# Kernel tuning notes

Measured on AMD Instinct MI355X. Metric: run time of the kernel, lower is better.

## Reference

```python
import jax, jax.numpy as jnp
import numpy as np
from jax import lax

B, NPB = 4, 100000
N = B * NPB
C_BEV, C = 256, 64
H = W = 180
S = 10          # NUM_SWEEPS
MAXI = 64       # gt_boxes.shape[1] (max instances per sample)
NUMLOC = B * MAXI * S
NUMINST = B * MAXI
PC_MIN = -54.0
CELL = 0.075 * 8  # voxel * bev_image_stride


def setup_inputs() -> dict:
    key = jax.random.key(0)
    ks = jax.random.split(key, 20)
    pb = jnp.repeat(jnp.arange(B), NPB).astype(jnp.float32)
    xy = jax.random.uniform(ks[0], (N, 2), minval=-54.0, maxval=53.9)
    z = jax.random.uniform(ks[1], (N, 1), minval=-5.0, maxval=2.9)
    extra = jax.random.uniform(ks[2], (N, 2))
    sweep = jax.random.randint(ks[3], (N, 1), 0, S).astype(jnp.float32)
    inst = jax.random.randint(ks[4], (N, 1), 0, MAXI).astype(jnp.float32)
    points = jnp.concatenate([pb[:, None], xy, z, extra, sweep, inst, inst], axis=1)
    sc = 0.05
    return {
        'points': points,
        'spatial_features_2d': jax.random.normal(ks[5], (B, C_BEV, H, W)),
        'conv_w': jax.random.normal(ks[6], (C, C_BEV, 3, 3)) * sc,
        'bn_gamma': jnp.ones((C,)), 'bn_beta': jnp.zeros((C,)),
        'w_seg': jax.random.normal(ks[7], (C, 3)) * sc, 'b_seg': jnp.zeros((3,)),
        'w_reg': jax.random.normal(ks[8], (C, 3)) * sc, 'b_reg': jnp.zeros((3,)),
        'w_emb': jax.random.normal(ks[9], (C, 2)) * sc, 'b_emb': jnp.zeros((2,)),
        'w_shape': jax.random.normal(ks[10], (3, C)) * sc, 'b_shape': jnp.zeros((C,)),
        'w_tf': jax.random.normal(ks[11], (2 * C + 6, 7)) * sc, 'b_tf': jnp.zeros((7,)),
        'w_mos': jax.random.normal(ks[12], (C + 6, 1)) * sc, 'b_mos': jnp.zeros((1,)),
    }


def _forward(points, spatial_features_2d, conv_w, bn_gamma, bn_beta,
             w_seg, b_seg, w_reg, b_reg, w_emb, b_emb,
             w_shape, b_shape, w_tf, b_tf, w_mos, b_mos):
    # ---- shared_conv: Conv3x3 (no bias) + BatchNorm2d (training stats) + ReLU
    y = lax.conv_general_dilated(spatial_features_2d, conv_w, (1, 1), 'SAME',
                                 dimension_numbers=('NCHW', 'OIHW', 'NCHW'))
    mu = y.mean(axis=(0, 2, 3), keepdims=True)
    var = y.var(axis=(0, 2, 3), keepdims=True)
    y = (y - mu) * lax.rsqrt(var + 1e-5)
    bev = jax.nn.relu(y * bn_gamma[None, :, None, None] + bn_beta[None, :, None, None])
    bev_hwc = jnp.transpose(bev, (0, 2, 3, 1))  # [B,H,W,C]

    # ---- bilinear gather of BEV features at point locations (vectorized over batch)
    pb = points[:, 0].astype(jnp.int32)
    px = (points[:, 1] - PC_MIN) / CELL
    py = (points[:, 2] - PC_MIN) / CELL
    x0 = jnp.clip(jnp.floor(px).astype(jnp.int32), 0, W - 1)
    x1 = jnp.clip(x0 + 1, 0, W - 1)
    y0 = jnp.clip(jnp.floor(py).astype(jnp.int32), 0, H - 1)
    y1 = jnp.clip(y0 + 1, 0, H - 1)
    x0f, x1f = x0.astype(px.dtype), x1.astype(px.dtype)
    y0f, y1f = y0.astype(py.dtype), y1.astype(py.dtype)
    Ia = bev_hwc[pb, y0, x0]
    Ib = bev_hwc[pb, y1, x0]
    Ic = bev_hwc[pb, y0, x1]
    Id = bev_hwc[pb, y1, x1]
    wa = ((x1f - px) * (y1f - py))[:, None]
    wb = ((x1f - px) * (py - y0f))[:, None]
    wc = ((px - x0f) * (y1f - py))[:, None]
    wd = ((px - x0f) * (py - y0f))[:, None]
    points_feat = Ia * wa + Ib * wb + Ic * wc + Id * wd  # [N, C]

    # ---- point heads (single Linear each, mid_c=None)
    points_cls_logit = points_feat @ w_seg + b_seg
    points_offset = points_feat @ w_reg + b_reg
    points_embedding = points_feat @ w_emb + b_emb

    # ---- instance / local aggregation (training branch; all points foreground)
    sweep = points[:, 6].astype(jnp.int32)
    inst = points[:, 7].astype(jnp.int32)
    seg = (pb * MAXI + inst) * S + sweep  # dense local id in [0, NUMLOC)
    cnt = jax.ops.segment_sum(jnp.ones((N,), points.dtype), seg, NUMLOC)
    nonempty = cnt > 0
    xyz = points[:, 1:4]
    centroid = jax.ops.segment_sum(xyz, seg, NUMLOC) / jnp.clip(cnt, 1.0)[:, None]
    centered = xyz - centroid[seg]

    shape_enc = jax.ops.segment_max(centered @ w_shape + b_shape, seg, NUMLOC)
    shape_enc = jnp.where(nonempty[:, None], shape_enc, 0.0)
    locals_feat = jax.ops.segment_max(points_feat, seg, NUMLOC)
    locals_feat = jnp.where(nonempty[:, None], locals_feat, 0.0)
    locals_feat = locals_feat + shape_enc  # [NUMLOC, C]

    inst_of_local = jnp.arange(NUMLOC, dtype=jnp.int32) // S
    sweep_of_local = jnp.arange(NUMLOC, dtype=jnp.int32) % S
    neg_inf = jnp.array(-jnp.inf, locals_feat.dtype)
    globals_feat = jax.ops.segment_max(
        jnp.where(nonempty[:, None], locals_feat, neg_inf), inst_of_local, NUMINST)
    inst_nonempty = jax.ops.segment_max(nonempty, inst_of_local, NUMINST)
    globals_feat = jnp.where(inst_nonempty[:, None], globals_feat, 0.0)

    max_sweep = jax.ops.segment_max(jnp.where(nonempty, sweep_of_local, -1), inst_of_local, NUMINST)
    min_sweep = jax.ops.segment_min(jnp.where(nonempty, sweep_of_local, S), inst_of_local, NUMINST)
    inst_ids = jnp.arange(NUMINST, dtype=jnp.int32)
    idx_max = jnp.clip(inst_ids * S + max_sweep, 0, NUMLOC - 1)
    idx_min = jnp.clip(inst_ids * S + min_sweep, 0, NUMLOC - 1)
    init_center = centroid[idx_min]    # [NUMINST, 3]
    target_center = centroid[idx_max]  # [NUMINST, 3]

    locals_cat = jnp.concatenate(
        [locals_feat, globals_feat[inst_of_local], centroid, target_center[inst_of_local]], axis=1)
    locals_tf = locals_cat @ w_tf + b_tf  # [NUMLOC, 7]
    inst_feat = jnp.concatenate([globals_feat, init_center, target_center], axis=1)
    inst_mos = inst_feat @ w_mos + b_mos  # [NUMINST, 1]

    return points_cls_logit, points_offset, points_embedding, locals_tf, inst_mos


def reference(points, spatial_features_2d, conv_w, bn_gamma, bn_beta,
              w_seg, b_seg, w_reg, b_reg, w_emb, b_emb,
              w_shape, b_shape, w_tf, b_tf, w_mos, b_mos):
    return _forward(points, spatial_features_2d, conv_w, bn_gamma, bn_beta,
                    w_seg, b_seg, w_reg, b_reg, w_emb, b_emb,
                    w_shape, b_shape, w_tf, b_tf, w_mos, b_mos)
```

## Files before the change

### kernel.cpp

```cpp
#include <hip/hip_runtime.h>

typedef __attribute__((ext_vector_type(8))) unsigned short u16x8;
typedef __attribute__((ext_vector_type(8))) short s16x8;
typedef __attribute__((ext_vector_type(4))) float f32x4;

#define NPTS 400000
#define HW 32400
#define WID 180
#define NCI 256
#define NCO 64
#define NSEG 2560
#define NINST 256
#define NBLK 500
#define PPB 800

__device__ __forceinline__ float bf2f(unsigned short u) {
  union { unsigned int i; float f; } v; v.i = ((unsigned int)u) << 16; return v.f;
}
__device__ __forceinline__ unsigned short f2bf(float f) {
  unsigned int u = __float_as_uint(f);
  return (unsigned short)((u + 0x7fffu + ((u >> 16) & 1u)) >> 16);
}

__device__ __forceinline__ void gld_lds16(const void* g, void* l) {
  __builtin_amdgcn_global_load_lds((const __attribute__((address_space(1))) void*)g,
                                   (__attribute__((address_space(3))) void*)l, 16, 0, 0);
}

__global__ __launch_bounds__(256) void k_transpose(const float* __restrict__ x,
                                                   unsigned short* __restrict__ xt) {
  const int bw = blockIdx.x;
  const int h = blockIdx.y, b = blockIdx.z;
  const int w0 = (bw >> 2) * 64, ci0 = (bw & 3) * 64;
  __shared__ float tile[64][68];
  const int t = threadIdx.x;
  const int a = t & 15, c4 = t >> 4;
  const int w4 = a * 4;
  const bool ldok = (w0 + w4) < WID;
#pragma unroll
  for (int it = 0; it < 4; ++it) {
    int ci = c4 + it * 16;
    float4 v = make_float4(0.f, 0.f, 0.f, 0.f);
    if (ldok) v = *(const float4*)(x + ((size_t)(b * NCI + ci0 + ci) * WID + h) * WID + w0 + w4);
    tile[w4 + 0][ci] = v.x;
    tile[w4 + 1][ci] = v.y;
    tile[w4 + 2][ci] = v.z;
    tile[w4 + 3][ci] = v.w;
  }
  __syncthreads();
  const int q = t & 7, r = t >> 3;
#pragma unroll
  for (int it = 0; it < 2; ++it) {
    int wl = r + it * 32;
    int w = w0 + wl;
    if (w >= WID) continue;
    const float* row = &tile[wl][q * 8];
    float4 lo = *(const float4*)(row);
    float4 hi = *(const float4*)(row + 4);
    u16x8 o;
    o[0] = f2bf(lo.x); o[1] = f2bf(lo.y); o[2] = f2bf(lo.z); o[3] = f2bf(lo.w);
    o[4] = f2bf(hi.x); o[5] = f2bf(hi.y); o[6] = f2bf(hi.z); o[7] = f2bf(hi.w);
    *(u16x8*)(xt + ((size_t)((b * WID + h) * WID + w)) * NCI + ci0 + q * 8) = o;
  }
}

__global__ void k_wreorg(const float* __restrict__ wt, unsigned short* __restrict__ wb) {
  int id = blockIdx.x * 256 + threadIdx.x;
  if (id >= 9 * 8 * 64 * 32) return;
  int cw = id & 31;
  int co = (id >> 5) & 63;
  int chunk = (id >> 11) & 7;
  int tap = id >> 14;
  int ci = chunk * 32 + cw;
  wb[id] = f2bf(wt[((size_t)co * 256 + ci) * 9 + tap]);
}

#define ROWB 6272
#define RBUF 25600
__global__ __launch_bounds__(256, 3) void k_conv_mfma(const unsigned short* __restrict__ xt,
                                                   const unsigned short* __restrict__ wb,
                                                   const float* __restrict__ zbuf,
                                                   unsigned short* __restrict__ y,
                                                   float* __restrict__ part) {
  const int wg = blockIdx.x;
  const int lin = (wg & 7) * 90 + (wg >> 3);
  const int h2 = lin % 90;
  const int t2 = lin / 90;
  const int wth = t2 & 1, b = t2 >> 1;
  const int h0 = h2 * 2;
  const int w0 = wth * 96;
  __shared__ unsigned char strip[2][RBUF];
  __shared__ float redS[2][2][2][16], redQ[2][2][2][16];
  const int tid = threadIdx.x;
  const int lane = tid & 63, wv = tid >> 6;
  const int mh = wv >> 1, nh = wv & 1;
  const int l15 = lane & 15, lk = lane >> 4;

  const char* srcs[7];
#pragma unroll
  for (int k = 0; k < 7; ++k) {
    int j = wv + k * 4;
    int g = j * 64 + lane;
    int pxlin = g >> 2, sub = g & 3;
    int row = pxlin / 98;
    int px = pxlin - row * 98;
    int hh = h0 + row - 1;
    int worig = w0 + px - 1;
    bool valid = (j < 25) && (pxlin < 392) &&
                 (hh >= 0) && (hh < WID) && (worig >= 0) && (worig < WID);
    int cig = sub ^ ((px >> 1) & 3);
    srcs[k] = valid
        ? (const char*)(xt + ((size_t)((b * WID + hh) * WID + worig)) * NCI + cig * 8)
        : (const char*)zbuf + lane * 16;
  }

  f32x4 acc[6][2];
#pragma unroll
  for (int i = 0; i < 6; ++i)
#pragma unroll
    for (int j = 0; j < 2; ++j) { acc[i][j][0] = 0.f; acc[i][j][1] = 0.f; acc[i][j][2] = 0.f; acc[i][j][3] = 0.f; }

  auto stage = [&](unsigned char* buf, int chunk) {
#pragma unroll
    for (int k = 0; k < 7; ++k) {
      int j = wv + k * 4;
      if (j >= 25) break;
      gld_lds16(srcs[k] + chunk * 64, buf + j * 1024);
    }
  };

  stage(strip[0], 0);
  asm volatile("s_waitcnt vmcnt(0)" ::: "memory");
  __syncthreads();

  const unsigned short* wco[2];
#pragma unroll
  for (int nf = 0; nf < 2; ++nf)
    wco[nf] = wb + (size_t)((nh * 2 + nf) * 16 + l15) * 32 + lk * 8;

  for (int chunk = 0; chunk < 8; ++chunk) {
    s16x8 bfr[9][2];
#pragma unroll
    for (int tap = 0; tap < 9; ++tap)
#pragma unroll
      for (int nf = 0; nf < 2; ++nf)
        bfr[tap][nf] = *(const s16x8*)(wco[nf] + (size_t)(tap * 8 + chunk) * 2048);
    if (chunk < 7) stage(strip[(chunk + 1) & 1], chunk + 1);
    const unsigned char* buf = strip[chunk & 1];
#pragma unroll
    for (int tap = 0; tap < 9; ++tap) {
      const int dh = tap / 3, dw = tap % 3;
      s16x8 afr[6];
#pragma unroll
      for (int i = 0; i < 6; ++i) {
        int wp = i * 16 + l15 + dw;
        int byte = (mh + dh) * ROWB + wp * 64 + ((lk ^ ((wp >> 1) & 3)) * 16);
        afr[i] = *(const s16x8*)(buf + byte);
      }
#pragma unroll
      for (int i = 0; i < 6; ++i)
#pragma unroll
        for (int nf = 0; nf < 2; ++nf)
          acc[i][nf] = __builtin_amdgcn_mfma_f32_16x16x32_bf16(afr[i], bfr[tap][nf], acc[i][nf], 0, 0, 0);
    }
    asm volatile("s_waitcnt vmcnt(0)" ::: "memory");
    __syncthreads();
  }

  const int r4 = lk * 4;
  const int hrow = h0 + mh;
  float s[2] = {0.f, 0.f}, q[2] = {0.f, 0.f};
#pragma unroll
  for (int i = 0; i < 6; ++i) {
#pragma unroll
    for (int nf = 0; nf < 2; ++nf) {
      int co = (nh * 2 + nf) * 16 + l15;
#pragma unroll
      for (int j = 0; j < 4; ++j) {
        int w = w0 + i * 16 + r4 + j;
        if (w < WID) {
          float v = acc[i][nf][j];
          y[((size_t)(b * HW) + hrow * WID + w) * 64 + co] = f2bf(v);
          s[nf] += v; q[nf] = fmaf(v, v, q[nf]);
        }
      }
    }
  }
#pragma unroll
  for (int nf = 0; nf < 2; ++nf) {
    s[nf] += __shfl_xor(s[nf], 16); s[nf] += __shfl_xor(s[nf], 32);
    q[nf] += __shfl_xor(q[nf], 16); q[nf] += __shfl_xor(q[nf], 32);
  }
  if (lk == 0) {
#pragma unroll
    for (int nf = 0; nf < 2; ++nf) { redS[mh][nh][nf][l15] = s[nf]; redQ[mh][nh][nf][l15] = q[nf]; }
  }
  __syncthreads();
  if (tid < 64) {
    int co = tid;
    int nhh = co >> 5, nff = (co >> 4) & 1, ll = co & 15;
    part[((size_t)wg * 64 + co) * 2 + 0] = redS[0][nhh][nff][ll] + redS[1][nhh][nff][ll];
    part[((size_t)wg * 64 + co) * 2 + 1] = redQ[0][nhh][nff][ll] + redQ[1][nhh][nff][ll];
  }
}

__global__ void k_bnparams(const float* __restrict__ part, const float* __restrict__ gamma,
                           const float* __restrict__ beta, float* __restrict__ ab) {
  const int t = threadIdx.x;
  float s = 0.f, ss = 0.f;
  for (int k = 0; k < 720; ++k) { s += part[((size_t)k * 64 + t) * 2]; ss += part[((size_t)k * 64 + t) * 2 + 1]; }
  float mu = s / 129600.f;
  float var = ss / 129600.f - mu * mu;
  float a = rsqrtf(var + 1e-5f) * gamma[t];
  ab[t * 2] = a; ab[t * 2 + 1] = beta[t] - mu * a;
}

__global__ __launch_bounds__(256) void k_points(const float* __restrict__ pts,
                         const unsigned short* __restrict__ y,
                         const float* __restrict__ ab,
                         unsigned short* __restrict__ pf) {
  const int gid = blockIdx.x * 256 + threadIdx.x;
  const int lane = gid & 63;
  const int wid = gid >> 6;
  const float sa = ab[lane * 2], sb = ab[lane * 2 + 1];
#pragma unroll
  for (int it = 0; it < 8; ++it) {
    int p = wid * 8 + it;
    const float* pr = pts + (size_t)p * 9;
    float pbf = pr[0], xx = pr[1], yy = pr[2];
    int b = (int)pbf;
    float px = (xx - (-54.0f)) / 0.6f;
    float py = (yy - (-54.0f)) / 0.6f;
    int x0 = (int)floorf(px); x0 = min(max(x0, 0), WID - 1);
    int x1 = min(x0 + 1, WID - 1);
    int y0 = (int)floorf(py); y0 = min(max(y0, 0), WID - 1);
    int y1 = min(y0 + 1, WID - 1);
    float x0f = (float)x0, x1f = (float)x1, y0f = (float)y0, y1f = (float)y1;
    float wa = (x1f - px) * (y1f - py);
    float wb = (x1f - px) * (py - y0f);
    float wc = (px - x0f) * (y1f - py);
    float wd = (px - x0f) * (py - y0f);
    int i00 = y0 * WID + x0;
    int dx = x1 - x0;
    int dy = (y1 - y0) * WID;
    const unsigned short* bb = y + ((size_t)b * HW) * 64 + lane;
    float Ia = fmaf(bf2f(bb[(size_t)i00 * 64]), sa, sb);             Ia = Ia > 0.f ? Ia : 0.f;
    float Ic = fmaf(bf2f(bb[(size_t)(i00 + dx) * 64]), sa, sb);      Ic = Ic > 0.f ? Ic : 0.f;
    float Ib = fmaf(bf2f(bb[(size_t)(i00 + dy) * 64]), sa, sb);      Ib = Ib > 0.f ? Ib : 0.f;
    float Id = fmaf(bf2f(bb[(size_t)(i00 + dy + dx) * 64]), sa, sb); Id = Id > 0.f ? Id : 0.f;
    float f = wa * Ia + wb * Ib + wc * Ic + wd * Id;
    pf[(size_t)p * 64 + lane] = f2bf(f);
  }
}

__global__ void k_heads(const unsigned short* __restrict__ pf,
                        const float* __restrict__ wseg, const float* __restrict__ bseg,
                        const float* __restrict__ wreg, const float* __restrict__ breg,
                        const float* __restrict__ wemb, const float* __restrict__ bemb,
                        float* __restrict__ ocls, float* __restrict__ ooff, float* __restrict__ oemb) {
  const int p = blockIdx.x * 256 + threadIdx.x;
  if (p >= NPTS) return;
  float a0 = bseg[0], a1 = bseg[1], a2 = bseg[2];
  float r0 = breg[0], r1 = breg[1], r2 = breg[2];
  float e0 = bemb[0], e1 = bemb[1];
  const u16x8* q = (const u16x8*)(pf + (size_t)p * 64);
#pragma unroll
  for (int g = 0; g < 8; ++g) {
    u16x8 v8 = q[g];
#pragma unroll
    for (int k = 0; k < 8; ++k) {
      int kk = g * 8 + k;
      float v = bf2f(v8[k]);
      a0 = fmaf(v, wseg[kk * 3 + 0], a0);
      a1 = fmaf(v, wseg[kk * 3 + 1], a1);
      a2 = fmaf(v, wseg[kk * 3 + 2], a2);
      r0 = fmaf(v, wreg[kk * 3 + 0], r0);
      r1 = fmaf(v, wreg[kk * 3 + 1], r1);
      r2 = fmaf(v, wreg[kk * 3 + 2], r2);
      e0 = fmaf(v, wemb[kk * 2 + 0], e0);
      e1 = fmaf(v, wemb[kk * 2 + 1], e1);
    }
  }
  ocls[p * 3 + 0] = a0; ocls[p * 3 + 1] = a1; ocls[p * 3 + 2] = a2;
  ooff[p * 3 + 0] = r0; ooff[p * 3 + 1] = r1; ooff[p * 3 + 2] = r2;
  oemb[p * 2 + 0] = e0; oemb[p * 2 + 1] = e1;
}

__global__ __launch_bounds__(256) void k_hist2(const float* __restrict__ pts,
                                               int* __restrict__ seg, int* __restrict__ rankp,
                                               int* __restrict__ bh) {
  __shared__ int lc[NSEG];
  const int t = threadIdx.x, blk = blockIdx.x;
  for (int i = t; i < NSEG; i += 256) lc[i] = 0;
  __syncthreads();
  const int p0 = blk * PPB;
  for (int i = t; i < PPB; i += 256) {
    int p = p0 + i;
    const float* pr = pts + (size_t)p * 9;
    int b = (int)pr[0];
    int sw = (int)pr[6];
    int ins = (int)pr[7];
    int s = (b * 64 + ins) * 10 + sw;
    seg[p] = s;
    rankp[p] = atomicAdd(&lc[s], 1);
  }
  __syncthreads();
  for (int i = t; i < NSEG; i += 256) bh[(size_t)blk * NSEG + i] = lc[i];
}

__global__ void k_scan2a(const int* __restrict__ bh, int* __restrict__ basebk,
                         int* __restrict__ tot) {
  const int s = blockIdx.x * 256 + threadIdx.x;
  int acc = 0;
  for (int b = 0; b < NBLK; ++b) {
    int v = bh[(size_t)b * NSEG + s];
    basebk[(size_t)b * NSEG + s] = acc;
    acc += v;
  }
  tot[s] = acc;
}

__global__ void k_scan2b(const int* __restrict__ tot, int* __restrict__ base,
                         int* __restrict__ cnt) {
  __shared__ int csum[256];
  const int t = threadIdx.x;
  int loc[10]; int run = 0;
#pragma unroll
  for (int k = 0; k < 10; ++k) { loc[k] = tot[t * 10 + k]; run += loc[k]; }
  csum[t] = run;
  __syncthreads();
  if (t == 0) {
    int a = 0;
    for (int i = 0; i < 256; ++i) { int v = csum[i]; csum[i] = a; a += v; }
  }
  __syncthreads();
  int acc = csum[t];
#pragma unroll
  for (int k = 0; k < 10; ++k) {
    int s = t * 10 + k;
    base[s] = acc; cnt[s] = loc[k];
    acc += loc[k];
  }
}

__global__ void k_scatter2(const int* __restrict__ seg, const int* __restrict__ rankp,
                           const int* __restrict__ base, const int* __restrict__ basebk,
                           int* __restrict__ order) {
  const int p = blockIdx.x * 256 + threadIdx.x;
  if (p < NPTS) {
    int s = seg[p];
    int blk = p / PPB;
    order[base[s] + basebk[(size_t)blk * NSEG + s] + rankp[p]] = p;
  }
}

__global__ __launch_bounds__(512) void k_seg(const int* __restrict__ cnt, const int* __restrict__ base,
                      const int* __restrict__ order, const float* __restrict__ pts,
                      const unsigned short* __restrict__ pf,
                      const float* __restrict__ wsh, const float* __restrict__ bsh,
                      float* __restrict__ lf, float* __restrict__ centroid,
                      int* __restrict__ nonempty) {
  const int s = blockIdx.x;
  const int t = threadIdx.x, lane = t & 63, wv = t >> 6;
  const int n = cnt[s], bs = base[s];
  float sx = 0.f, sy = 0.f, sz = 0.f;
  for (int i = t; i < n; i += 512) {
    int p = order[bs + i];
    const float* pr = pts + (size_t)p * 9;
    sx += pr[1]; sy += pr[2]; sz += pr[3];
  }
#pragma unroll
  for (int m = 32; m > 0; m >>= 1) {
    sx += __shfl_xor(sx, m); sy += __shfl_xor(sy, m); sz += __shfl_xor(sz, m);
  }
  __shared__ float red[3][8];
  __shared__ float csh[3];
  if (lane == 0) { red[0][wv] = sx; red[1][wv] = sy; red[2][wv] = sz; }
  __syncthreads();
  if (t == 0) {
    float dn = (float)max(n, 1);
    float ax = 0.f, ay = 0.f, az = 0.f;
#pragma unroll
    for (int k = 0; k < 8; ++k) { ax += red[0][k]; ay += red[1][k]; az += red[2][k]; }
    csh[0] = ax / dn; csh[1] = ay / dn; csh[2] = az / dn;
  }
  __syncthreads();
  const float cx = csh[0], cy = csh[1], cz = csh[2];
  const float w0 = wsh[lane], w1 = wsh[64 + lane], w2 = wsh[128 + lane], bb = bsh[lane];
  float smax = -INFINITY, lmax = -INFINITY;
  for (int i = wv; i < n; i += 8) {
    int p = order[bs + i];
    const float* pr = pts + (size_t)p * 9;
    float sv = fmaf(pr[1] - cx, w0, fmaf(pr[2] - cy, w1, fmaf(pr[3] - cz, w2, bb)));
    smax = fmaxf(smax, sv);
    lmax = fmaxf(lmax, bf2f(pf[(size_t)p * 64 + lane]));
  }
  __shared__ float rs[8][64], rl[8][64];
  rs[wv][lane] = smax; rl[wv][lane] = lmax;
  __syncthreads();
  if (wv == 0) {
#pragma unroll
    for (int k = 1; k < 8; ++k) {
      smax = fmaxf(smax, rs[k][lane]);
      lmax = fmaxf(lmax, rl[k][lane]);
    }
    bool ne = n > 0;
    lf[s * 64 + lane] = (ne ? lmax : 0.f) + (ne ? smax : 0.f);
    if (lane == 0) {
      nonempty[s] = ne ? 1 : 0;
      centroid[s * 3 + 0] = cx; centroid[s * 3 + 1] = cy; centroid[s * 3 + 2] = cz;
    }
  }
}

__global__ void k_glob(const float* __restrict__ lf, const int* __restrict__ ne,
                       const float* __restrict__ centroid,
                       const float* __restrict__ wmos, const float* __restrict__ bmos,
                       float* __restrict__ gf, float* __restrict__ tc, float* __restrict__ ic,
                       float* __restrict__ omos) {
  const int i = blockIdx.x;
  const int t = threadIdx.x;
  float g = -INFINITY;
  int maxsw = -1, minsw = 10;
  bool any = false;
#pragma unroll
  for (int s = 0; s < 10; ++s) {
    int idx = i * 10 + s;
    bool e = ne[idx] != 0;
    float v = lf[idx * 64 + t];
    g = fmaxf(g, e ? v : -INFINITY);
    if (e) { any = true; maxsw = s; minsw = min(minsw, s); }
  }
  float gv = any ? g : 0.f;
  gf[i * 64 + t] = gv;
  int idxmax = min(max(i * 10 + maxsw, 0), NSEG - 1);
  int idxmin = min(max(i * 10 + minsw, 0), NSEG - 1);
  float tcx = centroid[idxmax * 3 + 0], tcy = centroid[idxmax * 3 + 1], tcz = centroid[idxmax * 3 + 2];
  float icx = centroid[idxmin * 3 + 0], icy = centroid[idxmin * 3 + 1], icz = centroid[idxmin * 3 + 2];
  if (t == 0) {
    tc[i * 3 + 0] = tcx; tc[i * 3 + 1] = tcy; tc[i * 3 + 2] = tcz;
    ic[i * 3 + 0] = icx; ic[i * 3 + 1] = icy; ic[i * 3 + 2] = icz;
  }
  float r = gv * wmos[t];
#pragma unroll
  for (int m = 32; m > 0; m >>= 1) r += __shfl_xor(r, m);
  if (t == 0) {
    r += icx * wmos[64] + icy * wmos[65] + icz * wmos[66];
    r += tcx * wmos[67] + tcy * wmos[68] + tcz * wmos[69];
    omos[i] = r + bmos[0];
  }
}

__global__ void k_tf(const float* __restrict__ lf, const float* __restrict__ gf,
                     const float* __restrict__ centroid, const float* __restrict__ tc,
                     const float* __restrict__ wtf, const float* __restrict__ btf,
                     float* __restrict__ otf) {
  const int r = blockIdx.x * 256 + threadIdx.x;
  if (r >= NSEG) return;
  const int i = r / 10;
  float acc[7];
#pragma unroll
  for (int j = 0; j < 7; ++j) acc[j] = btf[j];
  for (int k = 0; k < 64; ++k) {
    float v = lf[r * 64 + k];
#pragma unroll
    for (int j = 0; j < 7; ++j) acc[j] = fmaf(v, wtf[k * 7 + j], acc[j]);
  }
  for (int k = 0; k < 64; ++k) {
    float v = gf[i * 64 + k];
#pragma unroll
    for (int j = 0; j < 7; ++j) acc[j] = fmaf(v, wtf[(64 + k) * 7 + j], acc[j]);
  }
#pragma unroll
  for (int c = 0; c < 3; ++c) {
    float v = centroid[r * 3 + c];
#pragma unroll
    for (int j = 0; j < 7; ++j) acc[j] = fmaf(v, wtf[(128 + c) * 7 + j], acc[j]);
  }
#pragma unroll
  for (int c = 0; c < 3; ++c) {
    float v = tc[i * 3 + c];
#pragma unroll
    for (int j = 0; j < 7; ++j) acc[j] = fmaf(v, wtf[(131 + c) * 7 + j], acc[j]);
  }
#pragma unroll
  for (int j = 0; j < 7; ++j) otf[r * 7 + j] = acc[j];
}

extern "C" void kernel_launch(void* const* d_in, const int* in_sizes, int n_in,
                              void* d_out, int out_size, void* d_ws, size_t ws_size,
                              hipStream_t stream) {
  const float* pts   = (const float*)d_in[0];
  const float* x     = (const float*)d_in[1];
  const float* convw = (const float*)d_in[2];
  const float* gamma = (const float*)d_in[3];
  const float* beta  = (const float*)d_in[4];
  const float* wseg  = (const float*)d_in[5];
  const float* bseg  = (const float*)d_in[6];
  const float* wreg  = (const float*)d_in[7];
  const float* breg  = (const float*)d_in[8];
  const float* wemb  = (const float*)d_in[9];
  const float* bemb  = (const float*)d_in[10];
  const float* wsh   = (const float*)d_in[11];
  const float* bsh   = (const float*)d_in[12];
  const float* wtf   = (const float*)d_in[13];
  const float* btf   = (const float*)d_in[14];
  const float* wmos  = (const float*)d_in[15];
  const float* bmos  = (const float*)d_in[16];

  float* out = (float*)d_out;
  float* o_cls = out;
  float* o_off = out + 1200000;
  float* o_emb = out + 2400000;
  float* o_tf  = out + 3200000;
  float* o_mos = out + 3217920;

  char* wsp = (char*)d_ws;
  size_t off = 0;
  auto alloc = [&](size_t bytes) -> void* {
    void* p = wsp + off;
    off = (off + bytes + 255) & ~(size_t)255;
    return p;
  };
  unsigned short* xt   = (unsigned short*)alloc((size_t)4 * WID * WID * NCI * 2);
  unsigned short* pf   = xt;
  unsigned short* wbuf = (unsigned short*)alloc((size_t)9 * 8 * 64 * 32 * 2);
  unsigned short* y    = (unsigned short*)alloc((size_t)4 * HW * 64 * 2);
  int*   seg      = (int*)alloc((size_t)NPTS * 4);
  int*   rankp    = (int*)alloc((size_t)NPTS * 4);
  int*   order    = (int*)alloc((size_t)NPTS * 4);
  int*   bh       = (int*)alloc((size_t)NBLK * NSEG * 4);
  int*   basebk   = (int*)alloc((size_t)NBLK * NSEG * 4);
  int*   tot      = (int*)alloc(NSEG * 4);
  int*   cnt      = (int*)alloc(NSEG * 4);
  int*   base     = (int*)alloc(NSEG * 4);
  float* part     = (float*)alloc((size_t)720 * 64 * 2 * 4);
  float* ab       = (float*)alloc(64 * 2 * 4);
  float* centroid = (float*)alloc(NSEG * 3 * 4);
  float* lf       = (float*)alloc(NSEG * 64 * 4);
  int*   nonem    = (int*)alloc(NSEG * 4);
  float* gf       = (float*)alloc(NINST * 64 * 4);
  float* tc       = (float*)alloc(NINST * 3 * 4);
  float* ic       = (float*)alloc(NINST * 3 * 4);
  float* zbuf     = (float*)alloc(2048);
  (void)ws_size; (void)n_in; (void)in_sizes; (void)out_size;

  hipMemsetAsync(zbuf, 0, 2048, stream);

  k_hist2<<<NBLK, 256, 0, stream>>>(pts, seg, rankp, bh);
  k_scan2a<<<10, 256, 0, stream>>>(bh, basebk, tot);
  k_scan2b<<<1, 256, 0, stream>>>(tot, base, cnt);
  k_scatter2<<<(NPTS + 255) / 256, 256, 0, stream>>>(seg, rankp, base, basebk, order);
  k_transpose<<<dim3(12, WID, 4), 256, 0, stream>>>(x, xt);
  k_wreorg<<<576, 256, 0, stream>>>(convw, wbuf);
  k_conv_mfma<<<720, 256, 0, stream>>>(xt, wbuf, zbuf, y, part);
  k_bnparams<<<1, 64, 0, stream>>>(part, gamma, beta, ab);
  k_points<<<12500, 256, 0, stream>>>(pts, y, ab, pf);
  k_heads<<<(NPTS + 255) / 256, 256, 0, stream>>>(pf, wseg, bseg, wreg, breg, wemb, bemb,
                                                  o_cls, o_off, o_emb);
  k_seg<<<NSEG, 512, 0, stream>>>(cnt, base, order, pts, pf, wsh, bsh, lf, centroid, nonem);
  k_glob<<<NINST, 64, 0, stream>>>(lf, nonem, centroid, wmos, bmos, gf, tc, ic, o_mos);
  k_tf<<<(NSEG + 255) / 256, 256, 0, stream>>>(lf, gf, centroid, tc, wtf, btf, o_tf);
}
```

Baseline: 299.5 us.

## Triple-buffer conv input strips, swizzle transpose LDS, parallelize BN reduction

```diff
diff --git a/kernel.cpp b/kernel.cpp
--- a/kernel.cpp
+++ b/kernel.cpp
@@ -42,10 +42,10 @@
     int ci = c4 + it * 16;
     float4 v = make_float4(0.f, 0.f, 0.f, 0.f);
     if (ldok) v = *(const float4*)(x + ((size_t)(b * NCI + ci0 + ci) * WID + h) * WID + w0 + w4);
-    tile[w4 + 0][ci] = v.x;
-    tile[w4 + 1][ci] = v.y;
-    tile[w4 + 2][ci] = v.z;
-    tile[w4 + 3][ci] = v.w;
+    tile[w4 + 0][ci ^ 0]  = v.x;
+    tile[w4 + 1][ci ^ 8]  = v.y;
+    tile[w4 + 2][ci ^ 16] = v.z;
+    tile[w4 + 3][ci ^ 24] = v.w;
   }
   __syncthreads();
   const int q = t & 7, r = t >> 3;
@@ -54,7 +54,7 @@
     int wl = r + it * 32;
     int w = w0 + wl;
     if (w >= WID) continue;
-    const float* row = &tile[wl][q * 8];
+    const float* row = &tile[wl][(q ^ (wl & 3)) * 8];
     float4 lo = *(const float4*)(row);
     float4 hi = *(const float4*)(row + 4);
     u16x8 o;
@@ -76,8 +76,8 @@
 }
 
 #define ROWB 6272
-#define RBUF 25600
-__global__ __launch_bounds__(256, 3) void k_conv_mfma(const unsigned short* __restrict__ xt,
+#define RBUF 26624
+__global__ __launch_bounds__(256, 2) void k_conv_mfma(const unsigned short* __restrict__ xt,
                                                    const unsigned short* __restrict__ wb,
                                                    const float* __restrict__ zbuf,
                                                    unsigned short* __restrict__ y,
@@ -89,7 +89,7 @@
   const int wth = t2 & 1, b = t2 >> 1;
   const int h0 = h2 * 2;
   const int w0 = wth * 96;
-  __shared__ unsigned char strip[2][RBUF];
+  __shared__ unsigned char strip[3][RBUF];
   __shared__ float redS[2][2][2][16], redQ[2][2][2][16];
   const int tid = threadIdx.x;
   const int lane = tid & 63, wv = tid >> 6;
@@ -97,6 +97,7 @@
   const int l15 = lane & 15, lk = lane >> 4;
 
   const char* srcs[7];
+  int dstrow[7];
 #pragma unroll
   for (int k = 0; k < 7; ++k) {
     int j = wv + k * 4;
@@ -112,6 +113,7 @@
     srcs[k] = valid
         ? (const char*)(xt + ((size_t)((b * WID + hh) * WID + worig)) * NCI + cig * 8)
         : (const char*)zbuf + lane * 16;
+    dstrow[k] = (j < 25) ? j : 25;
   }
 
   f32x4 acc[6][2];
@@ -122,16 +124,15 @@
 
   auto stage = [&](unsigned char* buf, int chunk) {
 #pragma unroll
-    for (int k = 0; k < 7; ++k) {
-      int j = wv + k * 4;
-      if (j >= 25) break;
-      gld_lds16(srcs[k] + chunk * 64, buf + j * 1024);
-    }
+    for (int k = 0; k < 7; ++k)
+      gld_lds16(srcs[k] + chunk * 64, buf + dstrow[k] * 1024);
   };
 
   stage(strip[0], 0);
-  asm volatile("s_waitcnt vmcnt(0)" ::: "memory");
-  __syncthreads();
+  stage(strip[1], 1);
+  asm volatile("s_waitcnt vmcnt(7)" ::: "memory");
+  __builtin_amdgcn_s_barrier();
+  __builtin_amdgcn_sched_barrier(0);
 
   const unsigned short* wco[2];
 #pragma unroll
@@ -145,8 +146,8 @@
 #pragma unroll
       for (int nf = 0; nf < 2; ++nf)
         bfr[tap][nf] = *(const s16x8*)(wco[nf] + (size_t)(tap * 8 + chunk) * 2048);
-    if (chunk < 7) stage(strip[(chunk + 1) & 1], chunk + 1);
-    const unsigned char* buf = strip[chunk & 1];
+    if (chunk < 6) stage(strip[(chunk + 2) % 3], chunk + 2);
+    const unsigned char* buf = strip[chunk % 3];
 #pragma unroll
     for (int tap = 0; tap < 9; ++tap) {
       const int dh = tap / 3, dw = tap % 3;
@@ -163,8 +164,9 @@
         for (int nf = 0; nf < 2; ++nf)
           acc[i][nf] = __builtin_amdgcn_mfma_f32_16x16x32_bf16(afr[i], bfr[tap][nf], acc[i][nf], 0, 0, 0);
     }
-    asm volatile("s_waitcnt vmcnt(0)" ::: "memory");
-    __syncthreads();
+    asm volatile("s_waitcnt vmcnt(7) lgkmcnt(0)" ::: "memory");
+    __builtin_amdgcn_s_barrier();
+    __builtin_amdgcn_sched_barrier(0);
   }
 
   const int r4 = lk * 4;
@@ -206,13 +208,24 @@
 
 __global__ void k_bnparams(const float* __restrict__ part, const float* __restrict__ gamma,
                            const float* __restrict__ beta, float* __restrict__ ab) {
+  __shared__ float ls[256], lss[256];
   const int t = threadIdx.x;
+  const int c = t & 63, g = t >> 6;
   float s = 0.f, ss = 0.f;
-  for (int k = 0; k < 720; ++k) { s += part[((size_t)k * 64 + t) * 2]; ss += part[((size_t)k * 64 + t) * 2 + 1]; }
-  float mu = s / 129600.f;
-  float var = ss / 129600.f - mu * mu;
-  float a = rsqrtf(var + 1e-5f) * gamma[t];
-  ab[t * 2] = a; ab[t * 2 + 1] = beta[t] - mu * a;
+  for (int k = g; k < 720; k += 4) {
+    s += part[((size_t)k * 64 + c) * 2];
+    ss += part[((size_t)k * 64 + c) * 2 + 1];
+  }
+  ls[t] = s; lss[t] = ss;
+  __syncthreads();
+  if (t < 64) {
+    s = ls[t] + ls[t + 64] + ls[t + 128] + ls[t + 192];
+    ss = lss[t] + lss[t + 64] + lss[t + 128] + lss[t + 192];
+    float mu = s / 129600.f;
+    float var = ss / 129600.f - mu * mu;
+    float a = rsqrtf(var + 1e-5f) * gamma[t];
+    ab[t * 2] = a; ab[t * 2 + 1] = beta[t] - mu * a;
+  }
 }
 
 __global__ __launch_bounds__(256) void k_points(const float* __restrict__ pts,
@@ -554,7 +567,7 @@
   k_transpose<<<dim3(12, WID, 4), 256, 0, stream>>>(x, xt);
   k_wreorg<<<576, 256, 0, stream>>>(convw, wbuf);
   k_conv_mfma<<<720, 256, 0, stream>>>(xt, wbuf, zbuf, y, part);
-  k_bnparams<<<1, 64, 0, stream>>>(part, gamma, beta, ab);
+  k_bnparams<<<1, 256, 0, stream>>>(part, gamma, beta, ab);
   k_points<<<12500, 256, 0, stream>>>(pts, y, ab, pf);
   k_heads<<<(NPTS + 255) / 256, 256, 0, stream>>>(pf, wseg, bseg, wreg, breg, wemb, bemb,
                                                   o_cls, o_off, o_emb);
```

New measurement: 333.2 us. +11.3%, slower.
